# Kernel optimization log

Hardware: AMD Instinct MI355X
Metric: run time of the kernel (lower is better)

The kernel has to match this reference:

```python
import jax, jax.numpy as jnp
import numpy as np
import math


def setup_inputs() -> dict:
    key = jax.random.key(0)
    k1, = jax.random.split(key, 1)
    B, C, N = 64, 128, 4096
    x = jax.random.normal(k1, (B, C, N), dtype=jnp.float32)
    return {
        "x": x,
        "log_peak_width": jnp.asarray(math.log(3.0), dtype=jnp.float32),
        "log_valley_width": jnp.asarray(math.log(3.0), dtype=jnp.float32),
    }


def reference(x, log_peak_width, log_valley_width):
    # x: (B, C, N)
    B, C, N = x.shape
    diff = jnp.diff(x, axis=-1)                      # (B, C, N-1)
    sign_change = jnp.sign(jnp.diff(diff, axis=-1))  # (B, C, N-2)

    # Torch code gathers ALL nonzero positions across (B, C) flattened and sums
    # one gaussian bump per occurrence. Equivalent, jit-friendly form: count
    # occurrences per center position, then weight one gaussian row per center.
    peak_counts = (sign_change < 0).sum(axis=(0, 1)).astype(x.dtype)    # (N-2,)
    valley_counts = (sign_change > 0).sum(axis=(0, 1)).astype(x.dtype)  # (N-2,)

    pos = jnp.arange(N, dtype=x.dtype)               # (N,)
    centers = jnp.arange(1, N - 1, dtype=x.dtype)    # (N-2,) : nonzero index + 1
    dist = pos[None, :] - centers[:, None]           # (N-2, N)

    g_peak = jnp.exp(-(dist / jnp.exp(log_peak_width)) ** 2)
    g_valley = jnp.exp(-(dist / jnp.exp(log_valley_width)) ** 2)
    vec = peak_counts @ g_peak + valley_counts @ g_valley  # (N,)

    attn = jnp.zeros_like(x) + vec                   # broadcast to (B, C, N)
    a_min, a_max = attn.min(), attn.max()
    return (attn - a_min) / (a_max - a_min + 1e-6)
```

## Files before the change

### kernel.cpp

```cpp
#include <hip/hip_runtime.h>

#define N_POS 4096
#define NJ 4094

__global__ __launch_bounds__(256) void count_kernel(
    const float* __restrict__ x,
    unsigned int* __restrict__ peak,
    unsigned int* __restrict__ valley,
    int rows_per_block)
{
    const int tid  = threadIdx.x;
    const int lane = tid & 63;
    const int j0   = blockIdx.x * 1024 + tid * 4;
    const int row0 = blockIdx.y * rows_per_block;

    unsigned int pk0 = 0, pk1 = 0, pk2 = 0, pk3 = 0;
    unsigned int vl0 = 0, vl1 = 0, vl2 = 0, vl3 = 0;

    for (int r = 0; r < rows_per_block; ++r) {
        const float* rowp = x + (size_t)(row0 + r) * N_POS;
        float4 a = *reinterpret_cast<const float4*>(rowp + j0);
        float n0 = __shfl_down(a.x, 1);
        float n1 = __shfl_down(a.y, 1);
        if (lane == 63) {
            if (j0 + 5 < N_POS) { n0 = rowp[j0 + 4]; n1 = rowp[j0 + 5]; }
            else                { n0 = 0.f;          n1 = 0.f; }
        }
        float d1, d2, s;
        d1 = a.y - a.x; d2 = a.z - a.y; s = d2 - d1;
        pk0 += (s < 0.f); vl0 += (s > 0.f);
        d1 = a.z - a.y; d2 = a.w - a.z; s = d2 - d1;
        pk1 += (s < 0.f); vl1 += (s > 0.f);
        d1 = a.w - a.z; d2 = n0 - a.w;  s = d2 - d1;
        pk2 += (s < 0.f); vl2 += (s > 0.f);
        d1 = n0 - a.w;  d2 = n1 - n0;   s = d2 - d1;
        pk3 += (s < 0.f); vl3 += (s > 0.f);
    }

    if (j0 + 0 < NJ) { atomicAdd(&peak[j0 + 0], pk0); atomicAdd(&valley[j0 + 0], vl0); }
    if (j0 + 1 < NJ) { atomicAdd(&peak[j0 + 1], pk1); atomicAdd(&valley[j0 + 1], vl1); }
    if (j0 + 2 < NJ) { atomicAdd(&peak[j0 + 2], pk2); atomicAdd(&valley[j0 + 2], vl2); }
    if (j0 + 3 < NJ) { atomicAdd(&peak[j0 + 3], pk3); atomicAdd(&valley[j0 + 3], vl3); }
}

__global__ __launch_bounds__(256) void vec_kernel(
    const unsigned int* __restrict__ peak,
    const unsigned int* __restrict__ valley,
    const float* __restrict__ log_pw,
    const float* __restrict__ log_vw,
    float* __restrict__ vec)
{
    int p = blockIdx.x * blockDim.x + threadIdx.x;
    if (p >= N_POS) return;

    float wp = __expf(log_pw[0]);
    float wv = __expf(log_vw[0]);
    float inv_p2 = 1.f / (wp * wp);
    float inv_v2 = 1.f / (wv * wv);
    int Rp = min(NJ, (int)ceilf(wp * 8.f) + 1);
    int Rv = min(NJ, (int)ceilf(wv * 8.f) + 1);

    float sum = 0.f;
    {
        int jlo = max(0, p - 1 - Rp), jhi = min(NJ - 1, p - 1 + Rp);
        for (int j = jlo; j <= jhi; ++j) {
            float dist = (float)(p - (j + 1));
            sum += (float)peak[j] * __expf(-dist * dist * inv_p2);
        }
    }
    {
        int jlo = max(0, p - 1 - Rv), jhi = min(NJ - 1, p - 1 + Rv);
        for (int j = jlo; j <= jhi; ++j) {
            float dist = (float)(p - (j + 1));
            sum += (float)valley[j] * __expf(-dist * dist * inv_v2);
        }
    }
    vec[p] = sum;
}

__global__ __launch_bounds__(256) void norm_kernel(
    const float* __restrict__ vec, float* __restrict__ nvec)
{
    __shared__ float smin[4], smax[4];
    const int tid = threadIdx.x;

    float lmin = 1e30f, lmax = -1e30f;
    for (int i = tid; i < N_POS; i += 256) {
        float v = vec[i];
        lmin = fminf(lmin, v);
        lmax = fmaxf(lmax, v);
    }
    for (int off = 32; off; off >>= 1) {
        lmin = fminf(lmin, __shfl_down(lmin, off));
        lmax = fmaxf(lmax, __shfl_down(lmax, off));
    }
    const int wave = tid >> 6;
    if ((tid & 63) == 0) { smin[wave] = lmin; smax[wave] = lmax; }
    __syncthreads();
    if (tid == 0) {
        smin[0] = fminf(fminf(smin[0], smin[1]), fminf(smin[2], smin[3]));
        smax[0] = fmaxf(fmaxf(smax[0], smax[1]), fmaxf(smax[2], smax[3]));
    }
    __syncthreads();
    const float vmin = smin[0];
    const float inv  = 1.f / (smax[0] - vmin + 1e-6f);
    for (int i = tid; i < N_POS; i += 256)
        nvec[i] = (vec[i] - vmin) * inv;
}

__global__ __launch_bounds__(256) void bcast_kernel(
    const float4* __restrict__ nvec4, float4* __restrict__ out4, int total4)
{
    int idx    = blockIdx.x * blockDim.x + threadIdx.x;
    int stride = gridDim.x * blockDim.x;
    for (int i = idx; i < total4; i += stride)
        out4[i] = nvec4[i & 1023];
}

extern "C" void kernel_launch(void* const* d_in, const int* in_sizes, int n_in,
                              void* d_out, int out_size, void* d_ws, size_t ws_size,
                              hipStream_t stream) {
    const float* x   = (const float*)d_in[0];
    const float* lpw = (const float*)d_in[1];
    const float* lvw = (const float*)d_in[2];
    float* out = (float*)d_out;

    unsigned int* peak   = (unsigned int*)d_ws;
    unsigned int* valley = peak + 4096;
    float* vec  = (float*)(valley + 4096);
    float* nvec = vec + 4096;

    const int rows = in_sizes[0] / N_POS;
    const int row_groups = 128;
    const int rows_per_block = rows / row_groups;

    hipMemsetAsync(d_ws, 0, 2 * 4096 * sizeof(unsigned int), stream);

    dim3 g1(4, row_groups);
    count_kernel<<<g1, 256, 0, stream>>>(x, peak, valley, rows_per_block);
    vec_kernel<<<N_POS / 256, 256, 0, stream>>>(peak, valley, lpw, lvw, vec);
    norm_kernel<<<1, 256, 0, stream>>>(vec, nvec);
    bcast_kernel<<<2048, 256, 0, stream>>>((const float4*)nvec, (float4*)out,
                                           out_size / 4);
}
```

Baseline: 294.2 us.

## Pack peak/valley counts, fuse vec and norm kernels, vector-load neighbors in count

```diff
diff --git a/kernel.cpp b/kernel.cpp
--- a/kernel.cpp
+++ b/kernel.cpp
@@ -2,94 +2,101 @@
 
 #define N_POS 4096
 #define NJ 4094
+#define RPB 32
 
 __global__ __launch_bounds__(256) void count_kernel(
     const float* __restrict__ x,
-    unsigned int* __restrict__ peak,
-    unsigned int* __restrict__ valley,
-    int rows_per_block)
+    unsigned int* __restrict__ cnt)
 {
-    const int tid  = threadIdx.x;
-    const int lane = tid & 63;
-    const int j0   = blockIdx.x * 1024 + tid * 4;
-    const int row0 = blockIdx.y * rows_per_block;
+    const int tid = threadIdx.x;
+    const int j0  = blockIdx.x * 1024 + tid * 4;
+    const size_t row0 = (size_t)blockIdx.y * RPB;
 
     unsigned int pk0 = 0, pk1 = 0, pk2 = 0, pk3 = 0;
     unsigned int vl0 = 0, vl1 = 0, vl2 = 0, vl3 = 0;
 
-    for (int r = 0; r < rows_per_block; ++r) {
-        const float* rowp = x + (size_t)(row0 + r) * N_POS;
-        float4 a = *reinterpret_cast<const float4*>(rowp + j0);
-        float n0 = __shfl_down(a.x, 1);
-        float n1 = __shfl_down(a.y, 1);
-        if (lane == 63) {
-            if (j0 + 5 < N_POS) { n0 = rowp[j0 + 4]; n1 = rowp[j0 + 5]; }
-            else                { n0 = 0.f;          n1 = 0.f; }
+    const float* base = x + row0 * N_POS + j0;
+    const bool tail = (j0 + 4 >= N_POS);
+
+    #pragma unroll 4
+    for (int r = 0; r < RPB; ++r) {
+        const float* rowp = base + (size_t)r * N_POS;
+        float4 a = *reinterpret_cast<const float4*>(rowp);
+        float n0 = 0.f, n1 = 0.f;
+        if (!tail) {
+            float2 b = *reinterpret_cast<const float2*>(rowp + 4);
+            n0 = b.x; n1 = b.y;
         }
-        float d1, d2, s;
-        d1 = a.y - a.x; d2 = a.z - a.y; s = d2 - d1;
+        float s;
+        s = (a.z - a.y) - (a.y - a.x);
         pk0 += (s < 0.f); vl0 += (s > 0.f);
-        d1 = a.z - a.y; d2 = a.w - a.z; s = d2 - d1;
+        s = (a.w - a.z) - (a.z - a.y);
         pk1 += (s < 0.f); vl1 += (s > 0.f);
-        d1 = a.w - a.z; d2 = n0 - a.w;  s = d2 - d1;
+        s = (n0 - a.w) - (a.w - a.z);
         pk2 += (s < 0.f); vl2 += (s > 0.f);
-        d1 = n0 - a.w;  d2 = n1 - n0;   s = d2 - d1;
+        s = (n1 - n0) - (n0 - a.w);
         pk3 += (s < 0.f); vl3 += (s > 0.f);
     }
 
-    if (j0 + 0 < NJ) { atomicAdd(&peak[j0 + 0], pk0); atomicAdd(&valley[j0 + 0], vl0); }
-    if (j0 + 1 < NJ) { atomicAdd(&peak[j0 + 1], pk1); atomicAdd(&valley[j0 + 1], vl1); }
-    if (j0 + 2 < NJ) { atomicAdd(&peak[j0 + 2], pk2); atomicAdd(&valley[j0 + 2], vl2); }
-    if (j0 + 3 < NJ) { atomicAdd(&peak[j0 + 3], pk3); atomicAdd(&valley[j0 + 3], vl3); }
+    if (j0 + 0 < NJ) atomicAdd(&cnt[j0 + 0], pk0 | (vl0 << 16));
+    if (j0 + 1 < NJ) atomicAdd(&cnt[j0 + 1], pk1 | (vl1 << 16));
+    if (j0 + 2 < NJ) atomicAdd(&cnt[j0 + 2], pk2 | (vl2 << 16));
+    if (j0 + 3 < NJ) atomicAdd(&cnt[j0 + 3], pk3 | (vl3 << 16));
 }
 
-__global__ __launch_bounds__(256) void vec_kernel(
-    const unsigned int* __restrict__ peak,
-    const unsigned int* __restrict__ valley,
+__global__ __launch_bounds__(1024) void vecnorm_kernel(
+    const unsigned int* __restrict__ cnt,
     const float* __restrict__ log_pw,
     const float* __restrict__ log_vw,
-    float* __restrict__ vec)
+    float* __restrict__ nvec)
 {
-    int p = blockIdx.x * blockDim.x + threadIdx.x;
-    if (p >= N_POS) return;
+    __shared__ float s_pk[NJ];
+    __shared__ float s_vl[NJ];
+    __shared__ float s_gp[257];
+    __shared__ float s_gv[257];
+    __shared__ float smin[16], smax[16];
 
-    float wp = __expf(log_pw[0]);
-    float wv = __expf(log_vw[0]);
-    float inv_p2 = 1.f / (wp * wp);
-    float inv_v2 = 1.f / (wv * wv);
-    int Rp = min(NJ, (int)ceilf(wp * 8.f) + 1);
-    int Rv = min(NJ, (int)ceilf(wv * 8.f) + 1);
+    const int tid = threadIdx.x;
+    const float wp = __expf(log_pw[0]);
+    const float wv = __expf(log_vw[0]);
+    const float ip2 = 1.f / (wp * wp);
+    const float iv2 = 1.f / (wv * wv);
+    const int Rp = min(128, (int)ceilf(wp * 8.f) + 1);
+    const int Rv = min(128, (int)ceilf(wv * 8.f) + 1);
 
-    float sum = 0.f;
-    {
-        int jlo = max(0, p - 1 - Rp), jhi = min(NJ - 1, p - 1 + Rp);
-        for (int j = jlo; j <= jhi; ++j) {
-            float dist = (float)(p - (j + 1));
-            sum += (float)peak[j] * __expf(-dist * dist * inv_p2);
+    for (int j = tid; j < NJ; j += 1024) {
+        unsigned int c = cnt[j];
+        s_pk[j] = (float)(c & 0xFFFFu);
+        s_vl[j] = (float)(c >> 16);
+    }
+    for (int d = tid; d < 257; d += 1024) {
+        float dd = (float)(d - 128);
+        s_gp[d] = __expf(-dd * dd * ip2);
+        s_gv[d] = __expf(-dd * dd * iv2);
+    }
+    __syncthreads();
+
+    float v[4];
+    float lmin = 1e30f, lmax = -1e30f;
+    #pragma unroll
+    for (int k = 0; k < 4; ++k) {
+        const int p = tid + k * 1024;
+        float sum = 0.f;
+        {
+            int clo = max(1, p - Rp), chi = min(NJ, p + Rp);
+            for (int c = clo; c <= chi; ++c)
+                sum += s_pk[c - 1] * s_gp[p - c + 128];
         }
+        {
+            int clo = max(1, p - Rv), chi = min(NJ, p + Rv);
+            for (int c = clo; c <= chi; ++c)
+                sum += s_vl[c - 1] * s_gv[p - c + 128];
+        }
+        v[k] = sum;
+        lmin = fminf(lmin, sum);
+        lmax = fmaxf(lmax, sum);
     }
-    {
-        int jlo = max(0, p - 1 - Rv), jhi = min(NJ - 1, p - 1 + Rv);
-        for (int j = jlo; j <= jhi; ++j) {
-            float dist = (float)(p - (j + 1));
-            sum += (float)valley[j] * __expf(-dist * dist * inv_v2);
-        }
-    }
-    vec[p] = sum;
-}
 
-__global__ __launch_bounds__(256) void norm_kernel(
-    const float* __restrict__ vec, float* __restrict__ nvec)
-{
-    __shared__ float smin[4], smax[4];
-    const int tid = threadIdx.x;
-
-    float lmin = 1e30f, lmax = -1e30f;
-    for (int i = tid; i < N_POS; i += 256) {
-        float v = vec[i];
-        lmin = fminf(lmin, v);
-        lmax = fmaxf(lmax, v);
-    }
     for (int off = 32; off; off >>= 1) {
         lmin = fminf(lmin, __shfl_down(lmin, off));
         lmax = fmaxf(lmax, __shfl_down(lmax, off));
@@ -98,14 +105,20 @@
     if ((tid & 63) == 0) { smin[wave] = lmin; smax[wave] = lmax; }
     __syncthreads();
     if (tid == 0) {
-        smin[0] = fminf(fminf(smin[0], smin[1]), fminf(smin[2], smin[3]));
-        smax[0] = fmaxf(fmaxf(smax[0], smax[1]), fmaxf(smax[2], smax[3]));
+        float mn = smin[0], mx = smax[0];
+        #pragma unroll
+        for (int i = 1; i < 16; ++i) {
+            mn = fminf(mn, smin[i]);
+            mx = fmaxf(mx, smax[i]);
+        }
+        smin[0] = mn; smax[0] = mx;
     }
     __syncthreads();
     const float vmin = smin[0];
     const float inv  = 1.f / (smax[0] - vmin + 1e-6f);
-    for (int i = tid; i < N_POS; i += 256)
-        nvec[i] = (vec[i] - vmin) * inv;
+    #pragma unroll
+    for (int k = 0; k < 4; ++k)
+        nvec[tid + k * 1024] = (v[k] - vmin) * inv;
 }
 
 __global__ __launch_bounds__(256) void bcast_kernel(
@@ -125,21 +138,16 @@
     const float* lvw = (const float*)d_in[2];
     float* out = (float*)d_out;
 
-    unsigned int* peak   = (unsigned int*)d_ws;
-    unsigned int* valley = peak + 4096;
-    float* vec  = (float*)(valley + 4096);
-    float* nvec = vec + 4096;
+    unsigned int* cnt = (unsigned int*)d_ws;
+    float* nvec = (float*)(cnt + 4096);
 
     const int rows = in_sizes[0] / N_POS;
-    const int row_groups = 128;
-    const int rows_per_block = rows / row_groups;
 
-    hipMemsetAsync(d_ws, 0, 2 * 4096 * sizeof(unsigned int), stream);
+    hipMemsetAsync(cnt, 0, 4096 * sizeof(unsigned int), stream);
 
-    dim3 g1(4, row_groups);
-    count_kernel<<<g1, 256, 0, stream>>>(x, peak, valley, rows_per_block);
-    vec_kernel<<<N_POS / 256, 256, 0, stream>>>(peak, valley, lpw, lvw, vec);
-    norm_kernel<<<1, 256, 0, stream>>>(vec, nvec);
+    dim3 g1(4, rows / RPB);
+    count_kernel<<<g1, 256, 0, stream>>>(x, cnt);
+    vecnorm_kernel<<<1, 1024, 0, stream>>>(cnt, lpw, lvw, nvec);
     bcast_kernel<<<2048, 256, 0, stream>>>((const float4*)nvec, (float4*)out,
                                            out_size / 4);
 }
```

New measurement: 266.7 us. -9.3%, faster.
